# Kernel optimization log

Hardware: AMD Instinct MI355X
Metric: run time of the kernel (lower is better)

Reference implementation:

```python
import jax, jax.numpy as jnp
import numpy as np

B, T, C, H, DI = 4, 1024, 1024, 16, 128
TAU = 1.0
LAMBDA_CONF = 0.1
SYS2_THR = 1.0


def _ln(x, w, b):
    mu = x.mean(-1, keepdims=True)
    var = x.var(-1, keepdims=True)
    return (x - mu) * jax.lax.rsqrt(var + 1e-5) * w + b


def setup_inputs() -> dict:
    key = jax.random.key(0)
    ks = jax.random.split(key, 16)
    s = lambda i, shape: jax.random.normal(ks[i], shape, jnp.float32) * 0.02
    return {
        "h": jax.random.normal(ks[0], (B, T, C), jnp.float32),
        "ln_w": jnp.ones((C,), jnp.float32), "ln_b": jnp.zeros((C,), jnp.float32),
        "w_q": s(1, (C, C)), "w_k": s(2, (C, C)), "w_v": s(3, (C, C)),
        "w_o": s(4, (C, C)), "b_o": jnp.zeros((C,), jnp.float32),
        "U": s(5, (C, DI)), "V": s(6, (DI, C)),
        "gamma_w": s(7, (C, 1)), "gamma_b": jnp.zeros((1,), jnp.float32),
        "mass_w": s(8, (C, 1)), "mass_b": jnp.zeros((1,), jnp.float32),
        "eps_w": s(9, (C, 1)), "eps_b": jnp.zeros((1,), jnp.float32),
        "lg_w1": s(10, (C, 4 * C)), "lg_b1": jnp.zeros((4 * C,), jnp.float32),
        "lg_w2": s(11, (4 * C, C)), "lg_b2": jnp.zeros((C,), jnp.float32),
        "mlp_w1": s(12, (C, 4 * C)), "mlp_b1": jnp.zeros((4 * C,), jnp.float32),
        "mlp_w2": s(13, (4 * C, C)), "mlp_b2": jnp.zeros((C,), jnp.float32),
    }


def reference(h, ln_w, ln_b, w_q, w_k, w_v, w_o, b_o, U, V,
              gamma_w, gamma_b, mass_w, mass_b, eps_w, eps_b,
              lg_w1, lg_b1, lg_w2, lg_b2, mlp_w1, mlp_b1, mlp_w2, mlp_b2):
    hd = C // H
    h_norm = _ln(h, ln_w, ln_b)

    # ---- HamiltonianAttention (conservative force field) ----
    q = (h_norm @ w_q).reshape(B, T, H, hd).transpose(0, 2, 1, 3)  # [B,H,T,hd]
    k = (h_norm @ w_k).reshape(B, T, H, hd).transpose(0, 2, 1, 3)
    v = (h_norm @ w_v).reshape(B, T, H, hd).transpose(0, 2, 1, 3)
    scores = jnp.einsum('bhqd,bhkd->bhqk', q, k) / (hd ** 0.5) / TAU
    attn = jax.nn.softmax(scores, axis=-1)
    force = jnp.einsum('bhqk,bhkd->bhqd', attn, v).transpose(0, 2, 1, 3).reshape(B, T, C)
    f_attn = force @ w_o + b_o

    # ---- total force, low-rank projection ----
    f_total = f_attn - LAMBDA_CONF * h_norm
    f_proj = f_total @ U                               # [B,T,DI]

    # ---- FSI (force stability index) ----
    h_mag = jnp.linalg.norm(h_norm, axis=-1)           # [B,T]
    f_mag = jnp.linalg.norm(f_proj, axis=-1)
    fsi = h_mag / (2.0 * f_mag + 1e-6)

    # ---- CognitiveGearbox: per-token mass / timestep ----
    mass = 1.0 + jax.nn.softplus(h @ mass_w + mass_b)  # [B,T,1], mass >= 1
    eps = jax.nn.sigmoid(h @ eps_w + eps_b)            # [B,T,1], eps in (0,1)
    gamma = jax.nn.sigmoid(h_norm @ gamma_w + gamma_b) # [B,T,1] damping gate

    # ---- fused AGI momentum recurrence: m_t = gamma_t*m_{t-1} + (eps_t/mass_t)*f_t ----
    def step(m, inps):
        f_t, g_t, e_t, ms_t = inps                     # [B,DI],[B,1],[B,1],[B,1]
        m = g_t * m + (e_t / ms_t) * f_t
        return m, m

    xs = (f_proj.transpose(1, 0, 2), gamma.transpose(1, 0, 2),
          eps.transpose(1, 0, 2), mass.transpose(1, 0, 2))
    m0 = jnp.zeros((B, DI), h.dtype)
    _, m_seq = jax.lax.scan(step, m0, xs)              # [T,B,DI]
    m_new = m_seq.transpose(1, 0, 2)                   # [B,T,DI]

    # ---- position update + system-2 correction + MLP ----
    velocity = m_new @ V                               # [B,T,C]
    h_new = h + eps * velocity
    hn2 = _ln(h_new, ln_w, ln_b)
    sys2 = jax.nn.gelu(hn2 @ lg_w1 + lg_b1, approximate=False) @ lg_w2 + lg_b2
    gate = jax.nn.sigmoid(mass - SYS2_THR)
    h_final = h_new + gate * sys2
    hn3 = _ln(h_final, ln_w, ln_b)
    h_final = h_final + (jax.nn.gelu(hn3 @ mlp_w1 + mlp_b1, approximate=False) @ mlp_w2 + mlp_b2)
    return (h_final, m_new, fsi)
```

## Files before the change

### kernel.cpp

```cpp
#include <hip/hip_runtime.h>
#include <hip/hip_bf16.h>
#include <math.h>

typedef __attribute__((ext_vector_type(8))) short bf16x8;
typedef __attribute__((ext_vector_type(4))) float f32x4;

#define DEVI __device__ __forceinline__

constexpr int B_ = 4, T_ = 1024, C_ = 1024, H_ = 16, HD_ = 64, DI_ = 128;
constexpr int NTOK = B_ * T_;
constexpr int C4 = 4 * C_;
constexpr int C3 = 3 * C_;
constexpr float LAMBDA_CONF = 0.1f;

DEVI short f2bf(float f) {
  unsigned u = __builtin_bit_cast(unsigned, f);
  u += 0x7fffu + ((u >> 16) & 1u);
  return (short)(u >> 16);
}
DEVI unsigned pk2(float a, float b) {
  return (unsigned)(unsigned short)f2bf(a) | ((unsigned)(unsigned short)f2bf(b) << 16);
}
DEVI float sigm(float x) { return 1.f / (1.f + __expf(-x)); }
DEVI float geluf(float x) { return 0.5f * x * (1.f + erff(x * 0.70710678118654752440f)); }

DEVI void gload16(const void* g, void* l) {
  __builtin_amdgcn_global_load_lds((const __attribute__((address_space(1))) unsigned*)g,
                                   (__attribute__((address_space(3))) unsigned*)l, 16, 0, 0);
}

template <int EPI>
DEVI void epi_store(void* Outp, const float* bias, const float* resid, const float* tokv,
                    int row, int col, int N, float v) {
  size_t idx = (size_t)row * N + col;
  if (EPI == 0) {
    ((float*)Outp)[idx] = v;
  } else if (EPI == 1) {
    ((short*)Outp)[idx] = f2bf(v);
  } else if (EPI == 2) {
    ((short*)Outp)[idx] = f2bf(v + bias[col] - LAMBDA_CONF * resid[idx]);
  } else if (EPI == 3) {
    ((float*)Outp)[idx] = resid[idx] + tokv[row] * v;
  } else if (EPI == 4) {
    float x = v + bias[col];
    ((short*)Outp)[idx] = f2bf(geluf(x));
  } else if (EPI == 5) {
    float x = v + bias[col];
    float g = sigm(tokv[row] - 1.f);
    ((float*)Outp)[idx] = resid[idx] + g * x;
  } else if (EPI == 6) {
    ((float*)Outp)[idx] = resid[idx] + v + bias[col];
  }
}

__global__ __launch_bounds__(256) void transpose_cvt(const float* __restrict__ W,
                                                     short* __restrict__ Wt, int K, int N) {
  __shared__ float s[32][33];
  int n0 = blockIdx.x * 32, k0 = blockIdx.y * 32;
  int tx = threadIdx.x & 31, ty = threadIdx.x >> 5;
#pragma unroll
  for (int i = 0; i < 4; i++)
    s[ty + i * 8][tx] = W[(size_t)(k0 + ty + i * 8) * N + n0 + tx];
  __syncthreads();
#pragma unroll
  for (int i = 0; i < 4; i++)
    Wt[(size_t)(n0 + ty + i * 8) * K + k0 + tx] = f2bf(s[tx][ty + i * 8]);
}

__global__ __launch_bounds__(256) void transpose_v(const short* __restrict__ QKV,
                                                   short* __restrict__ VT) {
  __shared__ short s[32][33];
  int bh = blockIdx.z;
  int b = bh >> 4, h = bh & 15;
  int t0 = blockIdx.x * 32, d0 = blockIdx.y * 32;
  int tx = threadIdx.x & 31, ty = threadIdx.x >> 5;
#pragma unroll
  for (int i = 0; i < 4; i++)
    s[ty + i * 8][tx] =
        QKV[(size_t)(b * T_ + t0 + ty + i * 8) * C3 + 2 * C_ + h * 64 + d0 + tx];
  __syncthreads();
#pragma unroll
  for (int i = 0; i < 4; i++)
    VT[((size_t)bh * 64 + d0 + ty + i * 8) * T_ + t0 + tx] = s[tx][ty + i * 8];
}

DEVI float blk_red(float v, volatile float* sm) {
  int lane = threadIdx.x & 63, wv = threadIdx.x >> 6;
#pragma unroll
  for (int o = 32; o; o >>= 1) v += __shfl_down(v, o);
  __syncthreads();
  if (lane == 0) sm[wv] = v;
  __syncthreads();
  return sm[0] + sm[1] + sm[2] + sm[3];
}

template <int FULL, int WF32>
__global__ __launch_bounds__(256) void ln_kernel(
    const float* __restrict__ X, const float* __restrict__ lnw, const float* __restrict__ lnb,
    float* __restrict__ Out, short* __restrict__ OutBf,
    const float* __restrict__ gw, const float* __restrict__ gb,
    const float* __restrict__ mw, const float* __restrict__ mb,
    const float* __restrict__ ew, const float* __restrict__ eb,
    float* __restrict__ gammaA, float* __restrict__ epsA, float* __restrict__ massA,
    float* __restrict__ coefA, float* __restrict__ hmagA) {
  __shared__ float sm[4];
  int tok = blockIdx.x;
  const float* x = X + (size_t)tok * C_;
  int t4 = threadIdx.x * 4;
  float4 xv = *(const float4*)&x[t4];
  float s = xv.x + xv.y + xv.z + xv.w;
  float ss = xv.x * xv.x + xv.y * xv.y + xv.z * xv.z + xv.w * xv.w;
  s = blk_red(s, sm);
  ss = blk_red(ss, sm);
  float mu = s * (1.f / C_);
  float var = ss * (1.f / C_) - mu * mu;
  float rs = rsqrtf(var + 1e-5f);
  float4 wv = *(const float4*)&lnw[t4];
  float4 bv = *(const float4*)&lnb[t4];
  float4 hn;
  hn.x = (xv.x - mu) * rs * wv.x + bv.x;
  hn.y = (xv.y - mu) * rs * wv.y + bv.y;
  hn.z = (xv.z - mu) * rs * wv.z + bv.z;
  hn.w = (xv.w - mu) * rs * wv.w + bv.w;
  if (WF32) *(float4*)&Out[(size_t)tok * C_ + t4] = hn;
  short4 ob;
  ob.x = f2bf(hn.x); ob.y = f2bf(hn.y); ob.z = f2bf(hn.z); ob.w = f2bf(hn.w);
  *(short4*)&OutBf[(size_t)tok * C_ + t4] = ob;
  if (FULL) {
    float4 gwv = *(const float4*)&gw[t4];
    float4 mwv = *(const float4*)&mw[t4];
    float4 ewv = *(const float4*)&ew[t4];
    float gd = hn.x * gwv.x + hn.y * gwv.y + hn.z * gwv.z + hn.w * gwv.w;
    float md = xv.x * mwv.x + xv.y * mwv.y + xv.z * mwv.z + xv.w * mwv.w;
    float ed = xv.x * ewv.x + xv.y * ewv.y + xv.z * ewv.z + xv.w * ewv.w;
    float h2 = hn.x * hn.x + hn.y * hn.y + hn.z * hn.z + hn.w * hn.w;
    gd = blk_red(gd, sm);
    md = blk_red(md, sm);
    ed = blk_red(ed, sm);
    h2 = blk_red(h2, sm);
    if (threadIdx.x == 0) {
      float g = sigm(gd + gb[0]);
      float xm = md + mb[0];
      float sp = (xm > 20.f) ? xm : log1pf(expf(xm));
      float msv = 1.f + sp;
      float epv = sigm(ed + eb[0]);
      gammaA[tok] = g;
      massA[tok] = msv;
      epsA[tok] = epv;
      coefA[tok] = epv / msv;
      hmagA[tok] = sqrtf(h2);
    }
  }
}

template <int EPI, int MT, int NT>
__global__ __launch_bounds__(512) void gemmP(
    const short* __restrict__ A, const short* __restrict__ Bt, void* __restrict__ Outp,
    const float* __restrict__ bias, const float* __restrict__ resid,
    const float* __restrict__ tokv, int M, int N, int K) {
  constexpr int BM = 4 * MT * 16;
  constexpr int BN = 2 * NT * 16;
  constexpr int CA = BM / 64;
  constexpr int CB = BN / 64;
  constexpr int LPT = CA + CB;
  __shared__ short As[3][BM][64];
  __shared__ short Bs[3][BN][64];
  int tid = threadIdx.x, lane = tid & 63, w = tid >> 6;
  int wr = w >> 1, wc = w & 1;
  int fr = lane & 15, fg = lane >> 4;
  int nMt = M / BM;
  int cpx = gridDim.x >> 3;
  int gbid = (blockIdx.x & 7) * cpx + (blockIdx.x >> 3);
  int chunk = gbid >> 5;
  int wi = gbid & 31;
  int nCM = nMt >> 2;
  int bm = ((chunk % nCM) * 4 + (wi & 3)) * BM;
  int bn = ((chunk / nCM) * 8 + (wi >> 2)) * BN;
  f32x4 acc[MT][NT] = {};

  int jsw = (lane & 7) ^ ((lane >> 3) & 7);
  const short* gA = A + (size_t)(bm + w * 8 + (lane >> 3)) * K + (jsw << 3);
  const short* gB = Bt + (size_t)(bn + w * 8 + (lane >> 3)) * K + (jsw << 3);

  auto stage = [&](int buf, int kt) {
#pragma unroll
    for (int c = 0; c < CA; c++)
      gload16(gA + (size_t)(c * 64) * K + kt, &As[buf][c * 64 + w * 8][0]);
#pragma unroll
    for (int c = 0; c < CB; c++)
      gload16(gB + (size_t)(c * 64) * K + kt, &Bs[buf][c * 64 + w * 8][0]);
  };

  int nt = K >> 6;
  stage(0, 0);
  if (nt > 1) stage(1, 64);
  for (int t = 0; t < nt; t++) {
    if (t + 1 < nt) {
      if constexpr (LPT == 6) asm volatile("s_waitcnt vmcnt(6)" ::: "memory");
      else asm volatile("s_waitcnt vmcnt(4)" ::: "memory");
    } else {
      asm volatile("s_waitcnt vmcnt(0)" ::: "memory");
    }
    __builtin_amdgcn_s_barrier();
    __builtin_amdgcn_sched_barrier(0);
    int nb = t + 2;
    if (nb < nt) stage(nb % 3, nb << 6);
    int cb = t % 3;
    short(*Ac)[64] = As[cb];
    short(*Bc)[64] = Bs[cb];
    bf16x8 af[MT], bv[NT / 2];
#pragma unroll
    for (int kh = 0; kh < 2; kh++) {
#pragma unroll
      for (int i = 0; i < MT; i++) {
        int row = wr * (MT * 16) + i * 16 + fr;
        af[i] = *(const bf16x8*)&Ac[row][((((kh << 2) | fg)) ^ (fr & 7)) << 3];
      }
#pragma unroll
      for (int nh = 0; nh < 2; nh++) {
#pragma unroll
        for (int j = 0; j < NT / 2; j++) {
          int row = wc * (NT * 16) + nh * (NT / 2) * 16 + j * 16 + fr;
          bv[j] = *(const bf16x8*)&Bc[row][((((kh << 2) | fg)) ^ (fr & 7)) << 3];
        }
#pragma unroll
        for (int i = 0; i < MT; i++)
#pragma unroll
          for (int j = 0; j < NT / 2; j++)
            acc[i][nh * (NT / 2) + j] = __builtin_amdgcn_mfma_f32_16x16x32_bf16(
                af[i], bv[j], acc[i][nh * (NT / 2) + j], 0, 0, 0);
      }
    }
  }

#pragma unroll
  for (int mi = 0; mi < MT; mi++) {
    int row0 = bm + wr * (MT * 16) + mi * 16 + fg * 4;
#pragma unroll
    for (int ni = 0; ni < NT; ni++) {
      int col = bn + wc * (NT * 16) + ni * 16 + fr;
#pragma unroll
      for (int r = 0; r < 4; r++)
        epi_store<EPI>(Outp, bias, resid, tokv, row0 + r, col, N, acc[mi][ni][r]);
    }
  }
}

template <int EPI>
__global__ __launch_bounds__(256) void gemm128(
    const short* __restrict__ A, const short* __restrict__ Bt, void* __restrict__ Outp,
    const float* __restrict__ bias, const float* __restrict__ resid,
    const float* __restrict__ tokv, int M, int N, int K) {
  __shared__ short As[3][128][32];
  __shared__ short Bs[3][128][32];
  int tid = threadIdx.x, lane = tid & 63, w = tid >> 6;
  int wr = w >> 1, wc = w & 1;
  int fr = lane & 15, fg = lane >> 4;
  int xm = (fr >> 1) & 3;
  int nM = M >> 7;
  int cpx = gridDim.x >> 3;
  int bid = (blockIdx.x & 7) * cpx + (blockIdx.x >> 3);
  int bm = (bid % nM) << 7;
  int bn = (bid / nM) << 7;
  f32x4 acc[4][4] = {};

  int jsw = (lane & 3) ^ ((lane >> 3) & 3);
  const short* gA = A + (size_t)(bm + w * 32 + (lane >> 2)) * K + (jsw << 3);
  const short* gB = Bt + (size_t)(bn + w * 32 + (lane >> 2)) * K + (jsw << 3);

  auto stage = [&](int buf, int kt) {
#pragma unroll
    for (int g = 0; g < 2; g++) {
      gload16(gA + (size_t)(g * 16) * K + kt, &As[buf][w * 32 + g * 16][0]);
      gload16(gB + (size_t)(g * 16) * K + kt, &Bs[buf][w * 32 + g * 16][0]);
    }
  };

  int nt = K >> 5;
  stage(0, 0);
  if (nt > 1) stage(1, 32);
  for (int t = 0; t < nt; t++) {
    if (t + 1 < nt) asm volatile("s_waitcnt vmcnt(4)" ::: "memory");
    else asm volatile("s_waitcnt vmcnt(0)" ::: "memory");
    __builtin_amdgcn_s_barrier();
    __builtin_amdgcn_sched_barrier(0);
    int nb = t + 2;
    if (nb < nt) stage(nb % 3, nb << 5);
    int cb = t % 3;
    bf16x8 af[4], bfv[4];
#pragma unroll
    for (int i = 0; i < 4; i++)
      af[i] = *(const bf16x8*)&As[cb][wr * 64 + i * 16 + fr][(fg ^ xm) << 3];
#pragma unroll
    for (int i = 0; i < 4; i++)
      bfv[i] = *(const bf16x8*)&Bs[cb][wc * 64 + i * 16 + fr][(fg ^ xm) << 3];
#pragma unroll
    for (int mi = 0; mi < 4; mi++)
#pragma unroll
      for (int ni = 0; ni < 4; ni++)
        acc[mi][ni] = __builtin_amdgcn_mfma_f32_16x16x32_bf16(af[mi], bfv[ni], acc[mi][ni], 0, 0, 0);
  }

#pragma unroll
  for (int mi = 0; mi < 4; mi++) {
    int row0 = bm + wr * 64 + mi * 16 + fg * 4;
#pragma unroll
    for (int ni = 0; ni < 4; ni++) {
      int col = bn + wc * 64 + ni * 16 + fr;
#pragma unroll
      for (int r = 0; r < 4; r++)
        epi_store<EPI>(Outp, bias, resid, tokv, row0 + r, col, N, acc[mi][ni][r]);
    }
  }
}

__global__ __launch_bounds__(256) void attn_kernel(const short* __restrict__ QKV,
                                                   const short* __restrict__ VT,
                                                   short* __restrict__ Fout) {
  __shared__ short Ks[2][64][64];
  __shared__ short Vts[2][64][64];
  __shared__ short Ps[4][16][72];
  int bh = blockIdx.y;
  int b = bh >> 4, h = bh & 15;
  int qt0 = blockIdx.x * 64;
  int tid = threadIdx.x, lane = tid & 63, w = tid >> 6;
  int fr = lane & 15, fg = lane >> 4;

  size_t base = ((size_t)b * T_) * C3 + h * 64;
  const short* Qp = QKV + base;
  const short* Kp = QKV + base + C_;
  const short* Vtp = VT + (size_t)bh * 64 * T_;
  int qrow = qt0 + w * 16 + fr;
  bf16x8 qf0 = *(const bf16x8*)&Qp[(size_t)qrow * C3 + fg * 8];
  bf16x8 qf1 = *(const bf16x8*)&Qp[(size_t)qrow * C3 + 32 + fg * 8];

  f32x4 oacc[4] = {};
  float m_run = -1e30f, l_run = 0.f;

  int jsw = (lane & 7) ^ ((lane >> 3) & 7);
  int sr8 = w * 8;
  int rsub = lane >> 3;

  auto stage = [&](int buf, int kt) {
#pragma unroll
    for (int c = 0; c < 2; c++) {
      int row = c * 32 + sr8 + rsub;
      gload16(Kp + (size_t)(kt + row) * C3 + jsw * 8, &Ks[buf][c * 32 + sr8][0]);
      gload16(Vtp + (size_t)row * T_ + kt + jsw * 8, &Vts[buf][c * 32 + sr8][0]);
    }
  };

  stage(0, 0);
  for (int t = 0; t < T_ / 64; t++) {
    if (t + 1 < T_ / 64) {
      stage((t + 1) & 1, (t + 1) * 64);
      asm volatile("s_waitcnt vmcnt(4)" ::: "memory");
    } else {
      asm volatile("s_waitcnt vmcnt(0)" ::: "memory");
    }
    __builtin_amdgcn_s_barrier();
    __builtin_amdgcn_sched_barrier(0);
    int cb = t & 1;

    f32x4 sacc[4];
#pragma unroll
    for (int kb = 0; kb < 4; kb++) {
      bf16x8 k0 = *(const bf16x8*)&Ks[cb][kb * 16 + fr][(fg ^ (fr & 7)) << 3];
      bf16x8 k1 = *(const bf16x8*)&Ks[cb][kb * 16 + fr][((4 | fg) ^ (fr & 7)) << 3];
      f32x4 z = {};
      z = __builtin_amdgcn_mfma_f32_16x16x32_bf16(k0, qf0, z, 0, 0, 0);
      z = __builtin_amdgcn_mfma_f32_16x16x32_bf16(k1, qf1, z, 0, 0, 0);
      sacc[kb] = z;
    }
    float mt = -1e30f;
#pragma unroll
    for (int kb = 0; kb < 4; kb++)
#pragma unroll
      for (int r = 0; r < 4; r++) {
        sacc[kb][r] *= 0.125f;
        mt = fmaxf(mt, sacc[kb][r]);
      }
    mt = fmaxf(mt, __shfl_xor(mt, 16));
    mt = fmaxf(mt, __shfl_xor(mt, 32));
    float m_new = fmaxf(m_run, mt);
    float alpha = __expf(m_run - m_new);
    float psum = 0.f;
    float pv[16];
#pragma unroll
    for (int kb = 0; kb < 4; kb++)
#pragma unroll
      for (int r = 0; r < 4; r++) {
        float p = __expf(sacc[kb][r] - m_new);
        pv[kb * 4 + r] = p;
        psum += p;
      }
    psum += __shfl_xor(psum, 16);
    psum += __shfl_xor(psum, 32);
    l_run = l_run * alpha + psum;
    m_run = m_new;

#pragma unroll
    for (int kb = 0; kb < 4; kb++) {
      uint2 pp;
      pp.x = pk2(pv[kb * 4 + 0], pv[kb * 4 + 1]);
      pp.y = pk2(pv[kb * 4 + 2], pv[kb * 4 + 3]);
      *(uint2*)&Ps[w][fr][kb * 16 + fg * 4] = pp;
    }
    float ar[4];
#pragma unroll
    for (int r = 0; r < 4; r++) ar[r] = __shfl(alpha, fg * 4 + r);
#pragma unroll
    for (int ni = 0; ni < 4; ni++)
#pragma unroll
      for (int r = 0; r < 4; r++) oacc[ni][r] *= ar[r];

    asm volatile("s_waitcnt lgkmcnt(0)" ::: "memory");
    __builtin_amdgcn_sched_barrier(0);
    bf16x8 pa0 = *(const bf16x8*)&Ps[w][fr][fg * 8];
    bf16x8 pa1 = *(const bf16x8*)&Ps[w][fr][32 + fg * 8];
#pragma unroll
    for (int ni = 0; ni < 4; ni++) {
      bf16x8 v0 = *(const bf16x8*)&Vts[cb][ni * 16 + fr][(fg ^ (fr & 7)) << 3];
      bf16x8 v1 = *(const bf16x8*)&Vts[cb][ni * 16 + fr][((4 | fg) ^ (fr & 7)) << 3];
      oacc[ni] = __builtin_amdgcn_mfma_f32_16x16x32_bf16(pa0, v0, oacc[ni], 0, 0, 0);
      oacc[ni] = __builtin_amdgcn_mfma_f32_16x16x32_bf16(pa1, v1, oacc[ni], 0, 0, 0);
    }
    __builtin_amdgcn_s_barrier();
  }

  float lr4[4];
#pragma unroll
  for (int r = 0; r < 4; r++) lr4[r] = __shfl(l_run, fg * 4 + r);
#pragma unroll
  for (int ni = 0; ni < 4; ni++)
#pragma unroll
    for (int r = 0; r < 4; r++) {
      int tok = b * T_ + qt0 + w * 16 + fg * 4 + r;
      Fout[(size_t)tok * C_ + h * 64 + ni * 16 + fr] = f2bf(oacc[ni][r] / lr4[r]);
    }
}

__global__ __launch_bounds__(128) void scan_kernel(const float* __restrict__ f_proj,
                                                   const float* __restrict__ gam,
                                                   const float* __restrict__ coef,
                                                   float* __restrict__ m_out,
                                                   short* __restrict__ m_bf) {
  int b = blockIdx.x;
  int d = threadIdx.x;
  const float* fp = f_proj + (size_t)b * T_ * DI_ + d;
  const float* g = gam + (size_t)b * T_;
  const float* c = coef + (size_t)b * T_;
  float* mo = m_out + (size_t)b * T_ * DI_ + d;
  short* mb = m_bf + (size_t)b * T_ * DI_ + d;
  float m = 0.f;
  for (int t = 0; t < T_; t += 8) {
    float fv[8], gv[8], cv[8];
#pragma unroll
    for (int i = 0; i < 8; i++) {
      fv[i] = fp[(size_t)(t + i) * DI_];
      gv[i] = g[t + i];
      cv[i] = c[t + i];
    }
#pragma unroll
    for (int i = 0; i < 8; i++) {
      m = gv[i] * m + cv[i] * fv[i];
      mo[(size_t)(t + i) * DI_] = m;
      mb[(size_t)(t + i) * DI_] = f2bf(m);
    }
  }
}

__global__ __launch_bounds__(256) void fsi_kernel(const float* __restrict__ f_proj,
                                                  const float* __restrict__ hmag,
                                                  float* __restrict__ fsi_out) {
  int tok = blockIdx.x * 4 + (threadIdx.x >> 6);
  int l = threadIdx.x & 63;
  float2 v = *(const float2*)&f_proj[(size_t)tok * DI_ + l * 2];
  float s = v.x * v.x + v.y * v.y;
#pragma unroll
  for (int o = 32; o; o >>= 1) s += __shfl_down(s, o);
  if (l == 0) fsi_out[tok] = hmag[tok] / (2.f * sqrtf(s) + 1e-6f);
}

extern "C" void kernel_launch(void* const* d_in, const int* in_sizes, int n_in,
                              void* d_out, int out_size, void* d_ws, size_t ws_size,
                              hipStream_t stream) {
  (void)in_sizes; (void)n_in; (void)out_size; (void)ws_size;
  const float* h = (const float*)d_in[0];
  const float* ln_w = (const float*)d_in[1];
  const float* ln_b = (const float*)d_in[2];
  const float* w_q = (const float*)d_in[3];
  const float* w_k = (const float*)d_in[4];
  const float* w_v = (const float*)d_in[5];
  const float* w_o = (const float*)d_in[6];
  const float* b_o = (const float*)d_in[7];
  const float* U = (const float*)d_in[8];
  const float* V = (const float*)d_in[9];
  const float* gamma_w = (const float*)d_in[10];
  const float* gamma_b = (const float*)d_in[11];
  const float* mass_w = (const float*)d_in[12];
  const float* mass_b = (const float*)d_in[13];
  const float* eps_w = (const float*)d_in[14];
  const float* eps_b = (const float*)d_in[15];
  const float* lg_w1 = (const float*)d_in[16];
  const float* lg_b1 = (const float*)d_in[17];
  const float* lg_w2 = (const float*)d_in[18];
  const float* lg_b2 = (const float*)d_in[19];
  const float* mlp_w1 = (const float*)d_in[20];
  const float* mlp_b1 = (const float*)d_in[21];
  const float* mlp_w2 = (const float*)d_in[22];
  const float* mlp_b2 = (const float*)d_in[23];

  float* out_h = (float*)d_out;
  float* out_m = out_h + (size_t)NTOK * C_;
  float* out_fsi = out_m + (size_t)NTOK * DI_;

  char* wsb = (char*)d_ws;
  size_t off = 0;
  auto al = [&](size_t bytes) {
    void* p = wsb + off;
    off += (bytes + 255) & ~(size_t)255;
    return p;
  };
  short* wqkvt = (short*)al((size_t)C3 * C_ * 2);
  short* wot = (short*)al((size_t)C_ * C_ * 2);
  short* ut = (short*)al((size_t)DI_ * C_ * 2);
  short* vt = (short*)al((size_t)C_ * DI_ * 2);
  short* lg1t = (short*)al((size_t)C4 * C_ * 2);
  short* lg2t = (short*)al((size_t)C_ * C4 * 2);
  short* mlp1t = (short*)al((size_t)C4 * C_ * 2);
  short* mlp2t = (short*)al((size_t)C_ * C4 * 2);
  float* h_norm = (float*)al((size_t)NTOK * C_ * 4);
  short* hn_bf = (short*)al((size_t)NTOK * C_ * 2);
  short* qkv_bf = (short*)al((size_t)NTOK * C3 * 2);
  short* tmp_bf = (short*)al((size_t)NTOK * C_ * 2);
  float* f_proj = (float*)al((size_t)NTOK * DI_ * 4);
  short* act = (short*)al((size_t)NTOK * C4 * 2);
  float* h_pre = (float*)al((size_t)NTOK * C_ * 4);
  short* vtrans = (short*)al((size_t)B_ * H_ * 64 * T_ * 2);
  float* gammaA = (float*)al((size_t)NTOK * 4);
  float* epsA = (float*)al((size_t)NTOK * 4);
  float* massA = (float*)al((size_t)NTOK * 4);
  float* coefA = (float*)al((size_t)NTOK * 4);
  float* hmagA = (float*)al((size_t)NTOK * 4);
  short* ftot_bf = hn_bf;
  short* m_bf = act;
  float* h_new = (float*)qkv_bf;

  dim3 blk(256);
  dim3 blk512(512);
  transpose_cvt<<<dim3(C_ / 32, C_ / 32), blk, 0, stream>>>(w_q, wqkvt, C_, C_);
  transpose_cvt<<<dim3(C_ / 32, C_ / 32), blk, 0, stream>>>(w_k, wqkvt + (size_t)C_ * C_, C_, C_);
  transpose_cvt<<<dim3(C_ / 32, C_ / 32), blk, 0, stream>>>(w_v, wqkvt + (size_t)2 * C_ * C_, C_, C_);
  transpose_cvt<<<dim3(C_ / 32, C_ / 32), blk, 0, stream>>>(w_o, wot, C_, C_);
  transpose_cvt<<<dim3(DI_ / 32, C_ / 32), blk, 0, stream>>>(U, ut, C_, DI_);
  transpose_cvt<<<dim3(C_ / 32, DI_ / 32), blk, 0, stream>>>(V, vt, DI_, C_);
  transpose_cvt<<<dim3(C4 / 32, C_ / 32), blk, 0, stream>>>(lg_w1, lg1t, C_, C4);
  transpose_cvt<<<dim3(C_ / 32, C4 / 32), blk, 0, stream>>>(lg_w2, lg2t, C4, C_);
  transpose_cvt<<<dim3(C4 / 32, C_ / 32), blk, 0, stream>>>(mlp_w1, mlp1t, C_, C4);
  transpose_cvt<<<dim3(C_ / 32, C4 / 32), blk, 0, stream>>>(mlp_w2, mlp2t, C4, C_);

  ln_kernel<1, 1><<<NTOK, blk, 0, stream>>>(h, ln_w, ln_b, h_norm, hn_bf, gamma_w, gamma_b,
                                            mass_w, mass_b, eps_w, eps_b, gammaA, epsA, massA,
                                            coefA, hmagA);
  gemmP<1, 4, 4><<<(NTOK / 256) * (C3 / 128), blk512, 0, stream>>>(hn_bf, wqkvt, qkv_bf, nullptr,
                                                                   nullptr, nullptr, NTOK, C3, C_);
  transpose_v<<<dim3(T_ / 32, 2, B_ * H_), blk, 0, stream>>>(qkv_bf, vtrans);
  attn_kernel<<<dim3(T_ / 64, B_ * H_), blk, 0, stream>>>(qkv_bf, vtrans, tmp_bf);
  gemmP<2, 2, 4><<<(NTOK / 128) * (C_ / 128), blk512, 0, stream>>>(tmp_bf, wot, ftot_bf, b_o,
                                                                   h_norm, nullptr, NTOK, C_, C_);
  gemm128<0><<<(NTOK / 128) * (DI_ / 128), blk, 0, stream>>>(ftot_bf, ut, f_proj, nullptr,
                                                             nullptr, nullptr, NTOK, DI_, C_);
  fsi_kernel<<<NTOK / 4, blk, 0, stream>>>(f_proj, hmagA, out_fsi);
  scan_kernel<<<B_, dim3(DI_), 0, stream>>>(f_proj, gammaA, coefA, out_m, m_bf);
  gemmP<3, 2, 4><<<(NTOK / 128) * (C_ / 128), blk512, 0, stream>>>(m_bf, vt, h_new, nullptr, h,
                                                                   epsA, NTOK, C_, DI_);
  ln_kernel<0, 0><<<NTOK, blk, 0, stream>>>(h_new, ln_w, ln_b, nullptr, tmp_bf, nullptr, nullptr,
                                            nullptr, nullptr, nullptr, nullptr, nullptr, nullptr,
                                            nullptr, nullptr, nullptr);
  gemmP<4, 4, 4><<<(NTOK / 256) * (C4 / 128), blk512, 0, stream>>>(tmp_bf, lg1t, act, lg_b1,
                                                                   nullptr, nullptr, NTOK, C4, C_);
  gemmP<5, 2, 4><<<(NTOK / 128) * (C_ / 128), blk512, 0, stream>>>(act, lg2t, h_pre, lg_b2,
                                                                   h_new, massA, NTOK, C_, C4);
  ln_kernel<0, 0><<<NTOK, blk, 0, stream>>>(h_pre, ln_w, ln_b, nullptr, tmp_bf, nullptr, nullptr,
                                            nullptr, nullptr, nullptr, nullptr, nullptr, nullptr,
                                            nullptr, nullptr, nullptr);
  gemmP<4, 4, 4><<<(NTOK / 256) * (C4 / 128), blk512, 0, stream>>>(tmp_bf, mlp1t, act, mlp_b1,
                                                                   nullptr, nullptr, NTOK, C4, C_);
  gemmP<6, 2, 4><<<(NTOK / 128) * (C_ / 128), blk512, 0, stream>>>(act, mlp2t, out_h, mlp_b2,
                                                                   h_pre, nullptr, NTOK, C_, C4);
}
```

Before: 540.2 us.

## Add 256x256-tile double-buffered GEMM for QKV and up-projection GEMMs

Adds a new GEMM kernel with 256x256 output tiles, 8 waves in a 2x4 layout, two LDS buffers, XOR-swizzled LDS layout and grouped tile rasterisation for L2 reuse. It replaces the 256x128-tile gemmP for the QKV projection and both 4C up-projection GEMMs. The larger tiles raise arithmetic intensity per LDS and global load. In exchange they need more registers (128 accumulators per lane), produce fewer blocks, and drop from triple to double buffering, which may expose more load latency.

```diff
diff --git a/kernel.cpp b/kernel.cpp
--- a/kernel.cpp
+++ b/kernel.cpp
@@ -153,6 +153,90 @@
   }
 }
 
+template <int EPI>
+__global__ __launch_bounds__(512, 2) void gemm256b(
+    const short* __restrict__ A, const short* __restrict__ Bt, void* __restrict__ Outp,
+    const float* __restrict__ bias, const float* __restrict__ resid,
+    const float* __restrict__ tokv, int M, int N, int K) {
+  __shared__ short As[2][256][64];
+  __shared__ short Bs[2][256][64];
+  int tid = threadIdx.x, lane = tid & 63, w = tid >> 6;
+  int wr = w >> 2, wc = w & 3;
+  int fr = lane & 15, fg = lane >> 4;
+  int nMt = M >> 8, nNt = N >> 8;
+  int cpx = gridDim.x >> 3;
+  int gbid = (blockIdx.x & 7) * cpx + (blockIdx.x >> 3);
+  int bm, bn;
+  if ((nNt & 7) == 0 && (nMt & 3) == 0) {
+    int chunk = gbid >> 5, wi = gbid & 31, nCM = nMt >> 2;
+    bm = ((chunk % nCM) * 4 + (wi & 3)) << 8;
+    bn = ((chunk / nCM) * 8 + (wi >> 2)) << 8;
+  } else {
+    bm = (gbid % nMt) << 8;
+    bn = (gbid / nMt) << 8;
+  }
+  f32x4 acc[8][4] = {};
+
+  int jsw = (lane & 7) ^ ((lane >> 3) & 7);
+  const short* gA = A + (size_t)(bm + w * 8 + (lane >> 3)) * K + (jsw << 3);
+  const short* gB = Bt + (size_t)(bn + w * 8 + (lane >> 3)) * K + (jsw << 3);
+
+  auto stage = [&](int buf, int kt) {
+#pragma unroll
+    for (int c = 0; c < 4; c++)
+      gload16(gA + (size_t)(c * 64) * K + kt, &As[buf][c * 64 + w * 8][0]);
+#pragma unroll
+    for (int c = 0; c < 4; c++)
+      gload16(gB + (size_t)(c * 64) * K + kt, &Bs[buf][c * 64 + w * 8][0]);
+  };
+
+  int nt = K >> 6;
+  stage(0, 0);
+  for (int t = 0; t < nt; t++) {
+    int cur = t & 1;
+    if (t + 1 < nt) {
+      stage(cur ^ 1, (t + 1) << 6);
+      asm volatile("s_waitcnt vmcnt(8)" ::: "memory");
+    } else {
+      asm volatile("s_waitcnt vmcnt(0)" ::: "memory");
+    }
+    __builtin_amdgcn_s_barrier();
+    __builtin_amdgcn_sched_barrier(0);
+    short(*Ac)[64] = As[cur];
+    short(*Bc)[64] = Bs[cur];
+#pragma unroll
+    for (int kh = 0; kh < 2; kh++) {
+      bf16x8 af[8], bv[4];
+#pragma unroll
+      for (int i = 0; i < 8; i++)
+        af[i] = *(const bf16x8*)&Ac[wr * 128 + i * 16 + fr][(((kh << 2) | fg) ^ (fr & 7)) << 3];
+#pragma unroll
+      for (int j = 0; j < 4; j++)
+        bv[j] = *(const bf16x8*)&Bc[wc * 64 + j * 16 + fr][(((kh << 2) | fg) ^ (fr & 7)) << 3];
+      __builtin_amdgcn_s_setprio(1);
+#pragma unroll
+      for (int i = 0; i < 8; i++)
+#pragma unroll
+        for (int j = 0; j < 4; j++)
+          acc[i][j] = __builtin_amdgcn_mfma_f32_16x16x32_bf16(af[i], bv[j], acc[i][j], 0, 0, 0);
+      __builtin_amdgcn_s_setprio(0);
+    }
+    __builtin_amdgcn_s_barrier();
+  }
+
+#pragma unroll
+  for (int mi = 0; mi < 8; mi++) {
+    int row0 = bm + wr * 128 + mi * 16 + fg * 4;
+#pragma unroll
+    for (int ni = 0; ni < 4; ni++) {
+      int col = bn + wc * 64 + ni * 16 + fr;
+#pragma unroll
+      for (int r = 0; r < 4; r++)
+        epi_store<EPI>(Outp, bias, resid, tokv, row0 + r, col, N, acc[mi][ni][r]);
+    }
+  }
+}
+
 template <int EPI, int MT, int NT>
 __global__ __launch_bounds__(512) void gemmP(
     const short* __restrict__ A, const short* __restrict__ Bt, void* __restrict__ Outp,
@@ -563,8 +647,8 @@
   ln_kernel<1, 1><<<NTOK, blk, 0, stream>>>(h, ln_w, ln_b, h_norm, hn_bf, gamma_w, gamma_b,
                                             mass_w, mass_b, eps_w, eps_b, gammaA, epsA, massA,
                                             coefA, hmagA);
-  gemmP<1, 4, 4><<<(NTOK / 256) * (C3 / 128), blk512, 0, stream>>>(hn_bf, wqkvt, qkv_bf, nullptr,
-                                                                   nullptr, nullptr, NTOK, C3, C_);
+  gemm256b<1><<<(NTOK / 256) * (C3 / 256), blk512, 0, stream>>>(hn_bf, wqkvt, qkv_bf, nullptr,
+                                                                nullptr, nullptr, NTOK, C3, C_);
   transpose_v<<<dim3(T_ / 32, 2, B_ * H_), blk, 0, stream>>>(qkv_bf, vtrans);
   attn_kernel<<<dim3(T_ / 64, B_ * H_), blk, 0, stream>>>(qkv_bf, vtrans, tmp_bf);
   gemmP<2, 2, 4><<<(NTOK / 128) * (C_ / 128), blk512, 0, stream>>>(tmp_bf, wot, ftot_bf, b_o,
@@ -578,15 +662,15 @@
   ln_kernel<0, 0><<<NTOK, blk, 0, stream>>>(h_new, ln_w, ln_b, nullptr, tmp_bf, nullptr, nullptr,
                                             nullptr, nullptr, nullptr, nullptr, nullptr, nullptr,
                                             nullptr, nullptr, nullptr);
-  gemmP<4, 4, 4><<<(NTOK / 256) * (C4 / 128), blk512, 0, stream>>>(tmp_bf, lg1t, act, lg_b1,
-                                                                   nullptr, nullptr, NTOK, C4, C_);
+  gemm256b<4><<<(NTOK / 256) * (C4 / 256), blk512, 0, stream>>>(tmp_bf, lg1t, act, lg_b1,
+                                                                nullptr, nullptr, NTOK, C4, C_);
   gemmP<5, 2, 4><<<(NTOK / 128) * (C_ / 128), blk512, 0, stream>>>(act, lg2t, h_pre, lg_b2,
                                                                    h_new, massA, NTOK, C_, C4);
   ln_kernel<0, 0><<<NTOK, blk, 0, stream>>>(h_pre, ln_w, ln_b, nullptr, tmp_bf, nullptr, nullptr,
                                             nullptr, nullptr, nullptr, nullptr, nullptr, nullptr,
                                             nullptr, nullptr, nullptr);
-  gemmP<4, 4, 4><<<(NTOK / 256) * (C4 / 128), blk512, 0, stream>>>(tmp_bf, mlp1t, act, mlp_b1,
-                                                                   nullptr, nullptr, NTOK, C4, C_);
+  gemm256b<4><<<(NTOK / 256) * (C4 / 256), blk512, 0, stream>>>(tmp_bf, mlp1t, act, mlp_b1,
+                                                                nullptr, nullptr, NTOK, C4, C_);
   gemmP<6, 2, 4><<<(NTOK / 128) * (C_ / 128), blk512, 0, stream>>>(act, mlp2t, out_h, mlp_b2,
                                                                    h_pre, nullptr, NTOK, C_, C4);
 }
```

After: 567.7 us. +5.1%, slower.

## Replace pipelined GEMMs with simple single-buffer 256-thread GEMM for QKV and MLPs

Applied to the files above, without the earlier changes.

Adds a new gemmS kernel: 256 threads, 128xNB tiles, BK=32, a single LDS buffer with a sync before and after each k-step, and XOR-swizzled fragment reads. It replaces the triple-buffered 512-thread gemmP in the QKV projection and both MLP pairs. For the down-projections the N tile shrinks to 64 to launch more blocks. The aim is higher occupancy (launch_bounds 256,3) and more blocks in flight, at the cost of losing the multi-stage load/compute overlap and issuing more global loads per flop.

```diff
diff --git a/kernel.cpp b/kernel.cpp
--- a/kernel.cpp
+++ b/kernel.cpp
@@ -153,6 +153,72 @@
   }
 }
 
+template <int EPI, int NB>
+__global__ __launch_bounds__(256, 3) void gemmS(
+    const short* __restrict__ A, const short* __restrict__ Bt, void* __restrict__ Outp,
+    const float* __restrict__ bias, const float* __restrict__ resid,
+    const float* __restrict__ tokv, int M, int N, int K) {
+  constexpr int NT = NB / 64;
+  constexpr int NFR = NB / 32;
+  __shared__ short As[128][32];
+  __shared__ short Bs[NB][32];
+  int tid = threadIdx.x, lane = tid & 63, w = tid >> 6;
+  int wr = w >> 1, wc = w & 1;
+  int fr = lane & 15, fg = lane >> 4;
+  int xm = (fr >> 1) & 3;
+  int nM = M >> 7;
+  int cpx = gridDim.x >> 3;
+  int bid = (blockIdx.x & 7) * cpx + (blockIdx.x >> 3);
+  int bm = (bid % nM) << 7;
+  int bn = (bid / nM) * NB;
+  f32x4 acc[4][NFR] = {};
+
+  int jsw = (lane & 3) ^ ((lane >> 3) & 3);
+  const short* gA = A + (size_t)(bm + w * 32 + (lane >> 2)) * K + (jsw << 3);
+  const short* gB;
+  if constexpr (NB == 128)
+    gB = Bt + (size_t)(bn + w * 32 + (lane >> 2)) * K + (jsw << 3);
+  else
+    gB = Bt + (size_t)(bn + w * 16 + (lane >> 2)) * K + (jsw << 3);
+
+  for (int kt = 0; kt < K; kt += 32) {
+    gload16(gA + kt, &As[w * 32][0]);
+    gload16(gA + (size_t)16 * K + kt, &As[w * 32 + 16][0]);
+    if constexpr (NB == 128) {
+      gload16(gB + kt, &Bs[w * 32][0]);
+      gload16(gB + (size_t)16 * K + kt, &Bs[w * 32 + 16][0]);
+    } else {
+      gload16(gB + kt, &Bs[w * 16][0]);
+    }
+    __syncthreads();
+    bf16x8 af[4], bv[NFR];
+#pragma unroll
+    for (int i = 0; i < 4; i++)
+      af[i] = *(const bf16x8*)&As[wr * 64 + i * 16 + fr][(fg ^ xm) << 3];
+#pragma unroll
+    for (int j = 0; j < NFR; j++)
+      bv[j] = *(const bf16x8*)&Bs[wc * (NB / 2) + j * 16 + fr][(fg ^ xm) << 3];
+#pragma unroll
+    for (int mi = 0; mi < 4; mi++)
+#pragma unroll
+      for (int ni = 0; ni < NFR; ni++)
+        acc[mi][ni] = __builtin_amdgcn_mfma_f32_16x16x32_bf16(af[mi], bv[ni], acc[mi][ni], 0, 0, 0);
+    __syncthreads();
+  }
+
+#pragma unroll
+  for (int mi = 0; mi < 4; mi++) {
+    int row0 = bm + wr * 64 + mi * 16 + fg * 4;
+#pragma unroll
+    for (int ni = 0; ni < NFR; ni++) {
+      int col = bn + wc * (NB / 2) + ni * 16 + fr;
+#pragma unroll
+      for (int r = 0; r < 4; r++)
+        epi_store<EPI>(Outp, bias, resid, tokv, row0 + r, col, N, acc[mi][ni][r]);
+    }
+  }
+}
+
 template <int EPI, int MT, int NT>
 __global__ __launch_bounds__(512) void gemmP(
     const short* __restrict__ A, const short* __restrict__ Bt, void* __restrict__ Outp,
@@ -563,8 +629,8 @@
   ln_kernel<1, 1><<<NTOK, blk, 0, stream>>>(h, ln_w, ln_b, h_norm, hn_bf, gamma_w, gamma_b,
                                             mass_w, mass_b, eps_w, eps_b, gammaA, epsA, massA,
                                             coefA, hmagA);
-  gemmP<1, 4, 4><<<(NTOK / 256) * (C3 / 128), blk512, 0, stream>>>(hn_bf, wqkvt, qkv_bf, nullptr,
-                                                                   nullptr, nullptr, NTOK, C3, C_);
+  gemmS<1, 128><<<(NTOK / 128) * (C3 / 128), blk, 0, stream>>>(hn_bf, wqkvt, qkv_bf, nullptr,
+                                                               nullptr, nullptr, NTOK, C3, C_);
   transpose_v<<<dim3(T_ / 32, 2, B_ * H_), blk, 0, stream>>>(qkv_bf, vtrans);
   attn_kernel<<<dim3(T_ / 64, B_ * H_), blk, 0, stream>>>(qkv_bf, vtrans, tmp_bf);
   gemmP<2, 2, 4><<<(NTOK / 128) * (C_ / 128), blk512, 0, stream>>>(tmp_bf, wot, ftot_bf, b_o,
@@ -578,15 +644,15 @@
   ln_kernel<0, 0><<<NTOK, blk, 0, stream>>>(h_new, ln_w, ln_b, nullptr, tmp_bf, nullptr, nullptr,
                                             nullptr, nullptr, nullptr, nullptr, nullptr, nullptr,
                                             nullptr, nullptr, nullptr);
-  gemmP<4, 4, 4><<<(NTOK / 256) * (C4 / 128), blk512, 0, stream>>>(tmp_bf, lg1t, act, lg_b1,
-                                                                   nullptr, nullptr, NTOK, C4, C_);
-  gemmP<5, 2, 4><<<(NTOK / 128) * (C_ / 128), blk512, 0, stream>>>(act, lg2t, h_pre, lg_b2,
-                                                                   h_new, massA, NTOK, C_, C4);
+  gemmS<4, 128><<<(NTOK / 128) * (C4 / 128), blk, 0, stream>>>(tmp_bf, lg1t, act, lg_b1,
+                                                               nullptr, nullptr, NTOK, C4, C_);
+  gemmS<5, 64><<<(NTOK / 128) * (C_ / 64), blk, 0, stream>>>(act, lg2t, h_pre, lg_b2,
+                                                             h_new, massA, NTOK, C_, C4);
   ln_kernel<0, 0><<<NTOK, blk, 0, stream>>>(h_pre, ln_w, ln_b, nullptr, tmp_bf, nullptr, nullptr,
                                             nullptr, nullptr, nullptr, nullptr, nullptr, nullptr,
                                             nullptr, nullptr, nullptr);
-  gemmP<4, 4, 4><<<(NTOK / 256) * (C4 / 128), blk512, 0, stream>>>(tmp_bf, mlp1t, act, mlp_b1,
-                                                                   nullptr, nullptr, NTOK, C4, C_);
-  gemmP<6, 2, 4><<<(NTOK / 128) * (C_ / 128), blk512, 0, stream>>>(act, mlp2t, out_h, mlp_b2,
-                                                                   h_pre, nullptr, NTOK, C_, C4);
-}
+  gemmS<4, 128><<<(NTOK / 128) * (C4 / 128), blk, 0, stream>>>(tmp_bf, mlp1t, act, mlp_b1,
+                                                               nullptr, nullptr, NTOK, C4, C_);
+  gemmS<6, 64><<<(NTOK / 128) * (C_ / 64), blk, 0, stream>>>(act, mlp2t, out_h, mlp_b2,
+                                                             h_pre, nullptr, NTOK, C_, C4);
+}
```

Measured after the change: 503.2 us. -6.8%, faster.
